# Kernel optimization log

Hardware: AMD Instinct MI355X
Metric: run time of the kernel (lower is better)

The kernel has to match this reference:

```python
import jax, jax.numpy as jnp
import numpy as np

D_MODEL, D_INNER, D_STATE, DT_RANK, D_CONV = 1024, 2048, 16, 64, 4
BATCH, SEQLEN = 2, 2048


def setup_inputs() -> dict:
    key = jax.random.key(0)
    ks = jax.random.split(key, 8)
    g = lambda k, shape, scale: jax.random.normal(k, shape, jnp.float32) * scale
    hidden_states = jax.random.normal(ks[0], (BATCH, SEQLEN, D_MODEL), jnp.float32)
    W_in = g(ks[1], (2 * D_INNER, D_MODEL), D_MODEL ** -0.5)
    conv_w = g(ks[2], (D_INNER, D_CONV), D_CONV ** -0.5)
    conv_b = jnp.zeros((D_INNER,), jnp.float32)
    W_x = g(ks[3], (DT_RANK + 2 * D_STATE, D_INNER), D_INNER ** -0.5)
    dt_init_std = DT_RANK ** -0.5  # dt_scale = 1.0
    W_dt = jax.random.uniform(ks[4], (D_INNER, DT_RANK), jnp.float32, -dt_init_std, dt_init_std)
    # faithful dt bias init: softplus^{-1}(dt) with dt ~ LogUniform(dt_min, dt_max)
    dt = jnp.exp(jax.random.uniform(ks[5], (D_INNER,), jnp.float32)
                 * (np.log(0.1) - np.log(0.001)) + np.log(0.001))
    dt = jnp.clip(dt, 1e-4)
    b_dt = dt + jnp.log(-jnp.expm1(-dt))
    A_log = jnp.log(jnp.broadcast_to(jnp.arange(1, D_STATE + 1, dtype=jnp.float32), (D_INNER, D_STATE)))
    D_param = jnp.ones((D_INNER,), jnp.float32)
    W_out = g(ks[6], (D_MODEL, D_INNER), D_INNER ** -0.5)
    return dict(hidden_states=hidden_states, W_in=W_in, conv_w=conv_w, conv_b=conv_b,
                W_x=W_x, W_dt=W_dt, b_dt=b_dt, A_log=A_log, D_param=D_param, W_out=W_out)


def reference(hidden_states, W_in, conv_w, conv_b, W_x, W_dt, b_dt, A_log, D_param, W_out):
    B_, L, _ = hidden_states.shape
    # in_proj (no bias) then split into x / gate z
    xz = jnp.einsum('bld,ed->ble', hidden_states, W_in)  # (B, L, 2*d_inner)
    x, z = jnp.split(xz, 2, axis=-1)
    # depthwise causal conv1d (padding = d_conv - 1, truncated to L)
    xp = jnp.pad(x, ((0, 0), (D_CONV - 1, 0), (0, 0)))
    xc = conv_b + sum(conv_w[:, k] * xp[:, k:k + L, :] for k in range(D_CONV))
    x = jax.nn.silu(xc)  # (B, L, d_inner)
    # input-dependent SSM params
    A = -jnp.exp(A_log)  # (d_inner, d_state)
    proj = jnp.einsum('bld,ed->ble', x, W_x)
    dt_lo, Bm, Cm = jnp.split(proj, [DT_RANK, DT_RANK + D_STATE], axis=-1)
    dt = jax.nn.softplus(jnp.einsum('blr,dr->bld', dt_lo, W_dt) + b_dt)  # (B, L, d_inner)
    # sequential selective scan: h = exp(dt*A)*h + dt*B*x ; y = C.h + D*x
    def step(h, inp):
        x_t, dt_t, B_t, C_t = inp  # (B,d), (B,d), (B,n), (B,n)
        dA = jnp.exp(dt_t[..., None] * A)                       # (B, d, n)
        h = dA * h + (dt_t * x_t)[..., None] * B_t[:, None, :]  # (B, d, n)
        y_t = jnp.einsum('bdn,bn->bd', h, C_t)
        return h, y_t

    h0 = jnp.zeros((B_, D_INNER, D_STATE), x.dtype)
    xs = (x.swapaxes(0, 1), dt.swapaxes(0, 1), Bm.swapaxes(0, 1), Cm.swapaxes(0, 1))
    _, ys = jax.lax.scan(step, h0, xs)
    y = ys.swapaxes(0, 1) + D_param * x
    y = y * jax.nn.silu(z)
    return jnp.einsum('bld,md->blm', y, W_out)
```

## Files before the change

### kernel.cpp

```cpp
#include <hip/hip_runtime.h>

typedef _Float16 f16;
typedef f16   f16x2 __attribute__((ext_vector_type(2)));
typedef f16   f16x4 __attribute__((ext_vector_type(4)));
typedef f16   f16x8 __attribute__((ext_vector_type(8)));
typedef float f32x2 __attribute__((ext_vector_type(2)));
typedef float f32x4 __attribute__((ext_vector_type(4)));

#define LOG2E 1.44269504088896f

__device__ __forceinline__ float fast_exp(float x) {
    return __builtin_amdgcn_exp2f(x * LOG2E);
}
__device__ __forceinline__ float silu_f(float x) {
    return x / (1.f + __builtin_amdgcn_exp2f(-LOG2E * x));
}
__device__ __forceinline__ float softplus_f(float x) {
    if (x > 16.f) return x;
    float e = __builtin_amdgcn_exp2f(x * LOG2E);
    return __builtin_amdgcn_logf(1.f + e) * 0.69314718056f;
}

__device__ __forceinline__ void gload_lds16(const void* g, void* l) {
    __builtin_amdgcn_global_load_lds((__attribute__((address_space(1))) void*)(g),
                                     (__attribute__((address_space(3))) void*)(l), 16, 0, 0);
}

__global__ __launch_bounds__(256) void cvt_all(const float* __restrict__ hidden, const float* __restrict__ W_in,
                                               const float* __restrict__ W_out, const float* __restrict__ W_dt,
                                               const float* __restrict__ W_x,
                                               f16* __restrict__ h16, f16* __restrict__ Win16,
                                               f16* __restrict__ Wout16, f16* __restrict__ Wdt16,
                                               f16* __restrict__ Wx16) {
    int i = blockIdx.x * 256 + threadIdx.x;
    const float* src;
    f16* dst;
    int idx;
    if (i < 1048576) { src = hidden; dst = h16; idx = i; }
    else if (i < 2097152) { src = W_in; dst = Win16; idx = i - 1048576; }
    else if (i < 2621440) { src = W_out; dst = Wout16; idx = i - 2097152; }
    else if (i < 2654208) { src = W_dt; dst = Wdt16; idx = i - 2621440; }
    else {
        int q = i - 2654208;
        int r = q >> 9;
        f32x4 v = {0.f, 0.f, 0.f, 0.f};
        if (r < 96) v = ((const f32x4*)W_x)[q];
        f16x4 o = {(f16)v[0], (f16)v[1], (f16)v[2], (f16)v[3]};
        ((f16x4*)Wx16)[q] = o;
        return;
    }
    f32x4 v = ((const f32x4*)src)[idx];
    f16x4 o = {(f16)v[0], (f16)v[1], (f16)v[2], (f16)v[3]};
    ((f16x4*)dst)[idx] = o;
}

__global__ void reduce_proj(const f16* __restrict__ Pws, float* __restrict__ proj,
                            f16* __restrict__ dtlo) {
    int i = blockIdx.x * 256 + threadIdx.x;
    int m = i >> 5, c0 = (i & 31) * 4;
    f32x4 s = {0.f, 0.f, 0.f, 0.f};
#pragma unroll
    for (int z = 0; z < 8; z++) {
        f16x4 p = *(const f16x4*)(Pws + (size_t)z * 4096 * 128 + (size_t)m * 128 + c0);
        s += (f32x4){(float)p[0], (float)p[1], (float)p[2], (float)p[3]};
    }
    *(f32x4*)(proj + (size_t)m * 128 + c0) = s;
    if (c0 < 64) {
        f16x4 o = {(f16)s[0], (f16)s[1], (f16)s[2], (f16)s[3]};
        *(f16x4*)(dtlo + (size_t)m * 64 + c0) = o;
    }
}

__global__ __launch_bounds__(1024) void gemm256(const f16* __restrict__ A, const f16* __restrict__ B,
                                                f16* __restrict__ C, int N, int K) {
    __shared__ f16 As[4][256 * 32];
    __shared__ f16 Bs[4][256 * 32];
    const int tid = threadIdx.x;
    const int w = tid >> 6, l = tid & 63;
    const int wr = w >> 2, wc = w & 3;
    const int lrow = l & 15, lkb = l >> 4;
    const int gpos = ((lkb ^ ((lrow >> 1) & 3)) * 8);
    const int bid = blockIdx.y * 16 + blockIdx.x;
    const int wg = (bid & 7) * 32 + (bid >> 3);
    const int mt = wg >> 4, nt = wg & 15;
    const int NT = K >> 5;

    f32x4 acc[4][4];
#pragma unroll
    for (int i = 0; i < 4; i++)
#pragma unroll
        for (int j = 0; j < 4; j++) acc[i][j] = (f32x4){0.f, 0.f, 0.f, 0.f};

    const int srow = w * 16 + (l >> 2);
    const int sgran = (l & 3) ^ ((l >> 3) & 3);
    const f16* Ag = A + (size_t)(mt * 256 + srow) * K + sgran * 8;
    const f16* Bg = B + (size_t)(nt * 256 + srow) * K + sgran * 8;

#define SCALL(s, kt, q)                                        \
    do {                                                       \
        if ((q) == 0) gload_lds16(Ag + (kt), &As[s][w * 512]); \
        if ((q) == 1) gload_lds16(Bg + (kt), &Bs[s][w * 512]); \
    } while (0)

    SCALL(0, 0, 0); SCALL(0, 0, 1);
    SCALL(1, 32, 0); SCALL(1, 32, 1);
    SCALL(2, 64, 0); SCALL(2, 64, 1);

    for (int t = 0; t < NT; ++t) {
        const f16* as = As[t & 3];
        const f16* bs = Bs[t & 3];
        const int pslot = (t + 3) & 3;
        const int pkt = ((t + 3 < NT) ? (t + 3) : (NT - 1)) * 32;

        asm volatile("s_waitcnt vmcnt(4)" ::: "memory");
        __builtin_amdgcn_sched_barrier(0);
        __builtin_amdgcn_s_barrier();
        __builtin_amdgcn_sched_barrier(0);

        f16x8 af[4], bf[4];
#pragma unroll
        for (int i = 0; i < 4; i++)
            af[i] = *(const f16x8*)&as[(wr * 64 + i * 16 + lrow) * 32 + gpos];
#pragma unroll
        for (int j = 0; j < 4; j++)
            bf[j] = *(const f16x8*)&bs[(wc * 64 + j * 16 + lrow) * 32 + gpos];
        SCALL(pslot, pkt, 0);
        SCALL(pslot, pkt, 1);
        __builtin_amdgcn_s_barrier();
        __builtin_amdgcn_sched_barrier(0);
        __builtin_amdgcn_s_setprio(1);
#pragma unroll
        for (int i = 0; i < 4; i++)
#pragma unroll
            for (int j = 0; j < 4; j++)
                acc[i][j] = __builtin_amdgcn_mfma_f32_16x16x32_f16(af[i], bf[j], acc[i][j], 0, 0, 0);
        __builtin_amdgcn_s_setprio(0);
    }
#undef SCALL

    const int orow = mt * 256 + wr * 64 + (l >> 4) * 4;
    const int ocol = nt * 256 + wc * 64 + lrow;
#pragma unroll
    for (int i = 0; i < 4; i++)
#pragma unroll
        for (int j = 0; j < 4; j++)
#pragma unroll
            for (int q = 0; q < 4; q++)
                C[(size_t)(orow + i * 16 + q) * N + ocol + j * 16] = (f16)acc[i][j][q];
}

__global__ __launch_bounds__(512) void gemm_o32(const f16* __restrict__ A, const f16* __restrict__ B,
                                                float* __restrict__ C, int N, int K) {
    __shared__ f16 As[4][128 * 32];
    __shared__ f16 Bs[4][128 * 32];
    const int tid = threadIdx.x;
    const int w = tid >> 6, l = tid & 63;
    const int wr = w >> 2, wc = w & 3;
    const int lrow = l & 15, lkb = l >> 4;
    const int gpos = ((lkb ^ ((lrow >> 1) & 3)) * 8);
    const int bid = blockIdx.y * 8 + blockIdx.x;
    const int wg = (bid & 7) * 32 + (bid >> 3);
    const int nt = wg & 7, mt = wg >> 3;
    const int NT = K >> 5;

    f32x4 acc[4][2];
#pragma unroll
    for (int i = 0; i < 4; i++)
#pragma unroll
        for (int j = 0; j < 2; j++) acc[i][j] = (f32x4){0.f, 0.f, 0.f, 0.f};

    const int srow = w * 16 + (l >> 2);
    const int sgran = (l & 3) ^ ((l >> 3) & 3);
    const f16* Ag = A + (size_t)(mt * 128 + srow) * K + sgran * 8;
    const f16* Bg = B + (size_t)(nt * 128 + srow) * K + sgran * 8;

#define QCALL(s, kt, q)                                        \
    do {                                                       \
        if ((q) == 0) gload_lds16(Ag + (kt), &As[s][w * 512]); \
        if ((q) == 1) gload_lds16(Bg + (kt), &Bs[s][w * 512]); \
    } while (0)

    QCALL(0, 0, 0); QCALL(0, 0, 1);
    QCALL(1, 32, 0); QCALL(1, 32, 1);
    QCALL(2, 64, 0); QCALL(2, 64, 1);

    for (int t = 0; t < NT; ++t) {
        const f16* as = As[t & 3];
        const f16* bs = Bs[t & 3];
        const int pslot = (t + 3) & 3;
        const int pkt = ((t + 3 < NT) ? (t + 3) : (NT - 1)) * 32;

        asm volatile("s_waitcnt vmcnt(4)" ::: "memory");
        __builtin_amdgcn_sched_barrier(0);
        __builtin_amdgcn_s_barrier();
        __builtin_amdgcn_sched_barrier(0);

        f16x8 af[4], bf[2];
#pragma unroll
        for (int i = 0; i < 4; i++)
            af[i] = *(const f16x8*)&as[(wr * 64 + i * 16 + lrow) * 32 + gpos];
#pragma unroll
        for (int j = 0; j < 2; j++)
            bf[j] = *(const f16x8*)&bs[(wc * 32 + j * 16 + lrow) * 32 + gpos];
        QCALL(pslot, pkt, 0);
        QCALL(pslot, pkt, 1);
        __builtin_amdgcn_s_barrier();
        __builtin_amdgcn_sched_barrier(0);
        __builtin_amdgcn_s_setprio(1);
#pragma unroll
        for (int i = 0; i < 4; i++)
#pragma unroll
            for (int j = 0; j < 2; j++)
                acc[i][j] = __builtin_amdgcn_mfma_f32_16x16x32_f16(af[i], bf[j], acc[i][j], 0, 0, 0);
        __builtin_amdgcn_s_setprio(0);
    }
#undef QCALL

    const int orow = mt * 128 + wr * 64 + (l >> 4) * 4;
    const int ocol = nt * 128 + wc * 32 + lrow;
#pragma unroll
    for (int i = 0; i < 4; i++)
#pragma unroll
        for (int j = 0; j < 2; j++)
#pragma unroll
            for (int q = 0; q < 4; q++)
                C[(size_t)(orow + i * 16 + q) * N + ocol + j * 16] = acc[i][j][q];
}

template <int EPI, typename OutT>
__global__ __launch_bounds__(256) void gemm_gl(const f16* __restrict__ A, const f16* __restrict__ B,
                                               OutT* __restrict__ C, const float* __restrict__ bias,
                                               int M, int N, int K, int kstep) {
    __shared__ f16 As[2][128 * 64];
    __shared__ f16 Bs[2][128 * 64];
    const int tid = threadIdx.x;
    const int w = tid >> 6, l = tid & 63;
    const int wm = (w >> 1) * 64, wn = (w & 1) * 64;
    const int lrow = l & 15, lkb = l >> 4;
    const int swzr = lrow & 7;
    const int gx = gridDim.x;
    const int nwg = gx * gridDim.y;
    const int bid = blockIdx.y * gx + blockIdx.x;
    const int wg = (bid & 7) * (nwg >> 3) + (bid >> 3);
    const int nt = wg % gx, mt = wg / gx;
    const int kbeg = blockIdx.z * kstep;
    const int NT = kstep >> 6;
    OutT* Cz = C + (size_t)blockIdx.z * M * N;

    f32x4 acc[4][4];
#pragma unroll
    for (int i = 0; i < 4; i++)
#pragma unroll
        for (int j = 0; j < 4; j++) acc[i][j] = (f32x4){0.f, 0.f, 0.f, 0.f};

    const int srow = w * 32 + (l >> 3);
    const int sgran = (l & 7) ^ (l >> 3);
    const f16* Ag = A + (size_t)(mt * 128 + srow) * K + sgran * 8 + kbeg;
    const f16* Bg = B + (size_t)(nt * 128 + srow) * K + sgran * 8 + kbeg;

#define STAGE128(s, kt)                                                         \
    do {                                                                        \
        _Pragma("unroll")                                                       \
        for (int i = 0; i < 4; ++i) {                                           \
            gload_lds16(Ag + (size_t)(i * 8) * K + (kt), &As[s][(w * 32 + i * 8) * 64]); \
            gload_lds16(Bg + (size_t)(i * 8) * K + (kt), &Bs[s][(w * 32 + i * 8) * 64]); \
        }                                                                       \
    } while (0)

    STAGE128(0, 0);
    __syncthreads();

    int cur = 0;
    for (int t = 0; t < NT; ++t) {
        if (t + 1 < NT) STAGE128(cur ^ 1, (t + 1) * 64);
#pragma unroll
        for (int kk = 0; kk < 64; kk += 32) {
            f16x8 af[4], bf[4];
            const int g = (kk >> 3) + lkb;
#pragma unroll
            for (int i = 0; i < 4; i++) {
                af[i] = *(const f16x8*)&As[cur][(wm + i * 16 + lrow) * 64 + ((g ^ swzr) * 8)];
                bf[i] = *(const f16x8*)&Bs[cur][(wn + i * 16 + lrow) * 64 + ((g ^ swzr) * 8)];
            }
#pragma unroll
            for (int i = 0; i < 4; i++)
#pragma unroll
                for (int j = 0; j < 4; j++)
                    acc[i][j] = __builtin_amdgcn_mfma_f32_16x16x32_f16(af[i], bf[j], acc[i][j], 0, 0, 0);
        }
        __syncthreads();
        cur ^= 1;
    }
#undef STAGE128

    const int orow = mt * 128 + wm + (l >> 4) * 4;
    const int ocol = nt * 128 + wn + lrow;
#pragma unroll
    for (int fm = 0; fm < 4; fm++)
#pragma unroll
        for (int fn = 0; fn < 4; fn++) {
            int c = ocol + fn * 16;
            float bv = (EPI == 1) ? bias[c] : 0.f;
#pragma unroll
            for (int i = 0; i < 4; i++) {
                float v = acc[fm][fn][i];
                if (EPI == 1) v = softplus_f(v + bv);
                Cz[(size_t)(orow + fm * 16 + i) * N + c] = (OutT)v;
            }
        }
}

__global__ __launch_bounds__(256) void conv_silu_k(const f16* __restrict__ xz, const float* __restrict__ cw,
                                                   const float* __restrict__ cb, f16* __restrict__ xc) {
    const int d0 = threadIdx.x * 8;
    const int g = blockIdx.x;
    const int b = g >> 9;
    const int l0 = (g & 511) * 4;
    const size_t mrow = (size_t)b * 2048 + l0;
    f32x4 cwv[8];
    float r0[8];
#pragma unroll
    for (int j = 0; j < 8; j++) {
        r0[j] = cb[d0 + j];
        cwv[j] = *(const f32x4*)(cw + (size_t)(d0 + j) * 4);
    }
    const f16x8 zero = {(f16)0.f, (f16)0.f, (f16)0.f, (f16)0.f, (f16)0.f, (f16)0.f, (f16)0.f, (f16)0.f};
    f16x8 xv[7];
#pragma unroll
    for (int i = 0; i < 7; ++i) {
        int ls = l0 - 3 + i;
        xv[i] = (ls >= 0) ? *(const f16x8*)(xz + (mrow - 3 + i) * 4096 + d0) : zero;
    }
#pragma unroll
    for (int tt = 0; tt < 4; ++tt) {
        float r[8];
#pragma unroll
        for (int j = 0; j < 8; j++) r[j] = r0[j];
#pragma unroll
        for (int k = 0; k < 4; k++)
#pragma unroll
            for (int j = 0; j < 8; j++) r[j] += cwv[j][k] * (float)xv[tt + k][j];
        f16x8 o;
#pragma unroll
        for (int j = 0; j < 8; j++) o[j] = (f16)silu_f(r[j]);
        *(f16x8*)(xc + (mrow + tt) * 2048 + d0) = o;
    }
}

#define CT 32
#define NCHUNK 64
#define NSTATE 65536

__global__ __launch_bounds__(64) void scan_p1(const f16* __restrict__ dt16, const f16* __restrict__ xc,
                                              const float* __restrict__ proj, const float* __restrict__ A_log,
                                              f16* __restrict__ Pbuf, f16* __restrict__ Hend) {
    __shared__ float du_s[CT][64];
    __shared__ float bq_s[CT][16];
    const int l = threadIdx.x;
    const int c = blockIdx.x, dgb = blockIdx.y, b = blockIdx.z;
    const int d_base = dgb << 6;
    const int d = d_base + l;
    const size_t mb = (size_t)b * 2048 + (size_t)c * CT;

    float a[16];
#pragma unroll
    for (int i = 0; i < 16; i += 4) {
        f32x4 av = *(const f32x4*)(A_log + (size_t)d * 16 + i);
#pragma unroll
        for (int k = 0; k < 4; ++k) a[i + k] = -fast_exp(av[k]) * LOG2E;
    }
#pragma unroll
    for (int i = 0; i < 4; ++i) {
        int idx = i * 64 + l, row = idx >> 3, j0 = (idx & 7) * 8;
        size_t r = mb + row;
        f16x8 dt8 = *(const f16x8*)(dt16 + r * 2048 + d_base + j0);
        f16x8 xc8 = *(const f16x8*)(xc + r * 2048 + d_base + j0);
#pragma unroll
        for (int k = 0; k < 8; ++k) {
            union { f16x2 h2; float f; } u;
            u.h2[0] = dt8[k];
            u.h2[1] = (f16)((float)dt8[k] * (float)xc8[k]);
            du_s[row][j0 + k] = u.f;
        }
    }
#pragma unroll
    for (int i = 0; i < 2; ++i) {
        int idx = i * 64 + l, row = idx >> 2, s4 = (idx & 3) * 4;
        *(f32x4*)&bq_s[row][s4] = *(const f32x4*)(proj + (mb + row) * 128 + 64 + s4);
    }
    __syncthreads();

    float h[16];
#pragma unroll
    for (int i = 0; i < 16; ++i) h[i] = 0.f;
    float sdt = 0.f;
#pragma unroll 2
    for (int t = 0; t < CT; ++t) {
        union { float f; f16x2 h2; } u;
        u.f = du_s[t][l];
        float dtv = (float)u.h2[0], uv = (float)u.h2[1];
        sdt += dtv;
        f32x4 B0 = *(const f32x4*)&bq_s[t][0];
        f32x4 B1 = *(const f32x4*)&bq_s[t][4];
        f32x4 B2 = *(const f32x4*)&bq_s[t][8];
        f32x4 B3 = *(const f32x4*)&bq_s[t][12];
#pragma unroll
        for (int i = 0; i < 4; ++i) {
            h[i]      = fmaf(__builtin_amdgcn_exp2f(dtv * a[i]),      h[i],      uv * B0[i]);
            h[i + 4]  = fmaf(__builtin_amdgcn_exp2f(dtv * a[i + 4]),  h[i + 4],  uv * B1[i]);
            h[i + 8]  = fmaf(__builtin_amdgcn_exp2f(dtv * a[i + 8]),  h[i + 8],  uv * B2[i]);
            h[i + 12] = fmaf(__builtin_amdgcn_exp2f(dtv * a[i + 12]), h[i + 12], uv * B3[i]);
        }
    }
    const size_t base = (size_t)c * NSTATE + ((size_t)((b << 11) + d) << 4);
    f16x8 P0, P1, E0, E1;
#pragma unroll
    for (int i = 0; i < 8; ++i) {
        P0[i] = (f16)__builtin_amdgcn_exp2f(a[i] * sdt);
        P1[i] = (f16)__builtin_amdgcn_exp2f(a[i + 8] * sdt);
        E0[i] = (f16)h[i];
        E1[i] = (f16)h[i + 8];
    }
    *(f16x8*)(Pbuf + base) = P0;
    *(f16x8*)(Pbuf + base + 8) = P1;
    *(f16x8*)(Hend + base) = E0;
    *(f16x8*)(Hend + base + 8) = E1;
}

__global__ __launch_bounds__(256) void scan_combine(const f16* __restrict__ Pbuf, const f16* __restrict__ Hend,
                                                    f16* __restrict__ Hinit) {
    int s = blockIdx.x * 256 + threadIdx.x;
    float h = 0.f;
#pragma unroll
    for (int c = 0; c < NCHUNK; c++) {
        size_t o = (size_t)c * NSTATE + s;
        Hinit[o] = (f16)h;
        h = fmaf((float)Pbuf[o], h, (float)Hend[o]);
    }
}

__global__ __launch_bounds__(64) void scan_p2(const f16* __restrict__ dt16, const f16* __restrict__ xc,
                                              const f16* __restrict__ xz, const float* __restrict__ proj,
                                              const float* __restrict__ A_log, const float* __restrict__ Dp,
                                              const f16* __restrict__ Hinit, f16* __restrict__ y16) {
    __shared__ f32x2 dg_s[CT][64];
    __shared__ float bq_s[CT][16];
    __shared__ float cq_s[CT][16];
    const int l = threadIdx.x;
    const int c = blockIdx.x, dgb = blockIdx.y, b = blockIdx.z;
    const int d_base = dgb << 6;
    const int d = d_base + l;
    const size_t mb = (size_t)b * 2048 + (size_t)c * CT;

    float a[16];
#pragma unroll
    for (int i = 0; i < 16; i += 4) {
        f32x4 av = *(const f32x4*)(A_log + (size_t)d * 16 + i);
#pragma unroll
        for (int k = 0; k < 4; ++k) a[i + k] = -fast_exp(av[k]) * LOG2E;
    }
#pragma unroll
    for (int i = 0; i < 4; ++i) {
        int idx = i * 64 + l, row = idx >> 3, j0 = (idx & 7) * 8;
        size_t r = mb + row;
        f16x8 dt8 = *(const f16x8*)(dt16 + r * 2048 + d_base + j0);
        f16x8 xc8 = *(const f16x8*)(xc + r * 2048 + d_base + j0);
        f16x8 xz8 = *(const f16x8*)(xz + r * 4096 + 2048 + d_base + j0);
        f32x4 dv0 = *(const f32x4*)(Dp + d_base + j0);
        f32x4 dv1 = *(const f32x4*)(Dp + d_base + j0 + 4);
#pragma unroll
        for (int k = 0; k < 8; ++k) {
            float dtv = (float)dt8[k], xv = (float)xc8[k];
            union { f16x2 h2; float f; } u;
            u.h2[0] = dt8[k];
            u.h2[1] = (f16)(dtv * xv);
            float sz = silu_f((float)xz8[k]);
            float Dv = (k < 4) ? dv0[k & 3] : dv1[k & 3];
            union { f16x2 h2; float f; } v;
            v.h2[0] = (f16)sz;
            v.h2[1] = (f16)(Dv * xv * sz);
            dg_s[row][j0 + k] = (f32x2){u.f, v.f};
        }
    }
#pragma unroll
    for (int i = 0; i < 2; ++i) {
        int idx = i * 64 + l, row = idx >> 2, s4 = (idx & 3) * 4;
        *(f32x4*)&bq_s[row][s4] = *(const f32x4*)(proj + (mb + row) * 128 + 64 + s4);
        *(f32x4*)&cq_s[row][s4] = *(const f32x4*)(proj + (mb + row) * 128 + 80 + s4);
    }
    const size_t base = (size_t)c * NSTATE + ((size_t)((b << 11) + d) << 4);
    f16x8 H0 = *(const f16x8*)(Hinit + base);
    f16x8 H1 = *(const f16x8*)(Hinit + base + 8);
    float h[16];
#pragma unroll
    for (int i = 0; i < 8; ++i) { h[i] = (float)H0[i]; h[i + 8] = (float)H1[i]; }
    __syncthreads();

#pragma unroll 2
    for (int t = 0; t < CT; ++t) {
        f32x2 dgv = dg_s[t][l];
        union { float f; f16x2 h2; } u;
        u.f = dgv[0];
        float dtv = (float)u.h2[0], uv = (float)u.h2[1];
        f32x4 B0 = *(const f32x4*)&bq_s[t][0];
        f32x4 B1 = *(const f32x4*)&bq_s[t][4];
        f32x4 B2 = *(const f32x4*)&bq_s[t][8];
        f32x4 B3 = *(const f32x4*)&bq_s[t][12];
        f32x4 C0 = *(const f32x4*)&cq_s[t][0];
        f32x4 C1 = *(const f32x4*)&cq_s[t][4];
        f32x4 C2 = *(const f32x4*)&cq_s[t][8];
        f32x4 C3 = *(const f32x4*)&cq_s[t][12];
        float yp0 = 0.f, yp1 = 0.f, yp2 = 0.f, yp3 = 0.f;
#pragma unroll
        for (int i = 0; i < 4; ++i) {
            h[i]      = fmaf(__builtin_amdgcn_exp2f(dtv * a[i]),      h[i],      uv * B0[i]);
            h[i + 4]  = fmaf(__builtin_amdgcn_exp2f(dtv * a[i + 4]),  h[i + 4],  uv * B1[i]);
            h[i + 8]  = fmaf(__builtin_amdgcn_exp2f(dtv * a[i + 8]),  h[i + 8],  uv * B2[i]);
            h[i + 12] = fmaf(__builtin_amdgcn_exp2f(dtv * a[i + 12]), h[i + 12], uv * B3[i]);
            yp0 = fmaf(h[i], C0[i], yp0);
            yp1 = fmaf(h[i + 4], C1[i], yp1);
            yp2 = fmaf(h[i + 8], C2[i], yp2);
            yp3 = fmaf(h[i + 12], C3[i], yp3);
        }
        float yp = (yp0 + yp1) + (yp2 + yp3);
        union { float f; f16x2 h2; } v;
        v.f = dgv[1];
        float yv = fmaf(yp, (float)v.h2[0], (float)v.h2[1]);
        y16[(mb + t) * 2048 + d] = (f16)yv;
    }
}

extern "C" void kernel_launch(void* const* d_in, const int* in_sizes, int n_in,
                              void* d_out, int out_size, void* d_ws, size_t ws_size,
                              hipStream_t stream) {
    const float* hidden = (const float*)d_in[0];
    const float* W_in   = (const float*)d_in[1];
    const float* conv_w = (const float*)d_in[2];
    const float* conv_b = (const float*)d_in[3];
    const float* W_x    = (const float*)d_in[4];
    const float* W_dt   = (const float*)d_in[5];
    const float* b_dt   = (const float*)d_in[6];
    const float* A_log  = (const float*)d_in[7];
    const float* D_par  = (const float*)d_in[8];
    const float* W_out  = (const float*)d_in[9];
    float* out = (float*)d_out;

    char* ws = (char*)d_ws;
    size_t off = 0;
    auto alloc = [&](size_t bytes) { void* p = ws + off; off += (bytes + 255) & ~(size_t)255; return p; };
    f16* h16     = (f16*)alloc(4096ull * 1024 * 2);
    f16* Win16   = (f16*)alloc(4096ull * 1024 * 2);
    f16* Wx16    = (f16*)alloc(128ull * 2048 * 2);
    f16* Wdt16   = (f16*)alloc(2048ull * 64 * 2);
    f16* Wout16  = (f16*)alloc(1024ull * 2048 * 2);
    f16* xz16    = (f16*)alloc(4096ull * 4096 * 2);
    f16* xc16    = (f16*)alloc(4096ull * 2048 * 2);
    float* proj  = (float*)alloc(4096ull * 128 * 4);
    f16* dtlo16  = (f16*)alloc(4096ull * 64 * 2);
    f16* dt16    = (f16*)alloc(4096ull * 2048 * 2);
    f16* y16     = (f16*)alloc(4096ull * 2048 * 2);
    f16* Pws     = (f16*)y16;
    f16* Pbuf16  = (f16*)h16;
    f16* Hend16  = (f16*)y16;
    f16* Hinit16 = (f16*)Win16;
    (void)ws_size; (void)in_sizes; (void)n_in; (void)out_size;

    cvt_all<<<10624, 256, 0, stream>>>(hidden, W_in, W_out, W_dt, W_x,
                                       h16, Win16, Wout16, Wdt16, Wx16);

    gemm256<<<dim3(16, 16), 1024, 0, stream>>>(h16, Win16, xz16, 4096, 1024);
    conv_silu_k<<<1024, 256, 0, stream>>>(xz16, conv_w, conv_b, xc16);
    gemm_gl<0, f16><<<dim3(1, 32, 8), 256, 0, stream>>>(xc16, Wx16, Pws, nullptr, 4096, 128, 2048, 256);
    reduce_proj<<<512, 256, 0, stream>>>(Pws, proj, dtlo16);
    gemm_gl<1, f16><<<dim3(16, 32, 1), 256, 0, stream>>>(dtlo16, Wdt16, dt16, b_dt, 4096, 2048, 64, 64);
    scan_p1<<<dim3(NCHUNK, 32, 2), 64, 0, stream>>>(dt16, xc16, proj, A_log, Pbuf16, Hend16);
    scan_combine<<<256, 256, 0, stream>>>(Pbuf16, Hend16, Hinit16);
    scan_p2<<<dim3(NCHUNK, 32, 2), 64, 0, stream>>>(dt16, xc16, xz16, proj, A_log, D_par, Hinit16, y16);
    gemm_o32<<<dim3(8, 32), 512, 0, stream>>>(y16, Wout16, out, 1024, 2048);
}
```

Baseline: 175.7 us.

## Split scan_p2 state dimension across 4 lanes with DPP reduction

Rewrites the second scan pass so each channel's 16 SSM states are spread over 4 lanes (4 states each), with blocks of 128 threads covering 32 channels and twice as many blocks in the grid. Partial C·h sums are combined across the 4 lanes with two DPP adds, and only one lane writes each output. This is meant to raise parallelism and occupancy and cut per-thread register pressure in the latency-bound recurrence. The cost is redundant exp/dt work and DPP overhead per lane, and only a quarter of the lanes doing the stores. It also pads the shared-memory arrays in both scan passes to reduce bank conflicts.

```diff
diff --git a/kernel.cpp b/kernel.cpp
--- a/kernel.cpp
+++ b/kernel.cpp
@@ -20,6 +20,9 @@
     float e = __builtin_amdgcn_exp2f(x * LOG2E);
     return __builtin_amdgcn_logf(1.f + e) * 0.69314718056f;
 }
+
+#define DPP_ADD(x, ctrl) \
+    ((x) + __int_as_float(__builtin_amdgcn_update_dpp(0, __float_as_int(x), (ctrl), 0xF, 0xF, true)))
 
 __device__ __forceinline__ void gload_lds16(const void* g, void* l) {
     __builtin_amdgcn_global_load_lds((__attribute__((address_space(1))) void*)(g),
@@ -354,7 +357,7 @@
 __global__ __launch_bounds__(64) void scan_p1(const f16* __restrict__ dt16, const f16* __restrict__ xc,
                                               const float* __restrict__ proj, const float* __restrict__ A_log,
                                               f16* __restrict__ Pbuf, f16* __restrict__ Hend) {
-    __shared__ float du_s[CT][64];
+    __shared__ float du_s[CT][66];
     __shared__ float bq_s[CT][16];
     const int l = threadIdx.x;
     const int c = blockIdx.x, dgb = blockIdx.y, b = blockIdx.z;
@@ -439,33 +442,31 @@
     }
 }
 
-__global__ __launch_bounds__(64) void scan_p2(const f16* __restrict__ dt16, const f16* __restrict__ xc,
-                                              const f16* __restrict__ xz, const float* __restrict__ proj,
-                                              const float* __restrict__ A_log, const float* __restrict__ Dp,
-                                              const f16* __restrict__ Hinit, f16* __restrict__ y16) {
-    __shared__ f32x2 dg_s[CT][64];
-    __shared__ float bq_s[CT][16];
-    __shared__ float cq_s[CT][16];
-    const int l = threadIdx.x;
-    const int c = blockIdx.x, dgb = blockIdx.y, b = blockIdx.z;
-    const int d_base = dgb << 6;
-    const int d = d_base + l;
+__global__ __launch_bounds__(128) void scan_p2(const f16* __restrict__ dt16, const f16* __restrict__ xc,
+                                               const f16* __restrict__ xz, const float* __restrict__ proj,
+                                               const float* __restrict__ A_log, const float* __restrict__ Dp,
+                                               const f16* __restrict__ Hinit, f16* __restrict__ y16) {
+    __shared__ f32x2 dg_s[CT][33];
+    __shared__ float bq_s[CT][20];
+    __shared__ float cq_s[CT][20];
+    const int tid = threadIdx.x;
+    const int c = blockIdx.x, dg = blockIdx.y, b = blockIdx.z;
+    const int d_base = dg << 5;
+    const int g = tid >> 2, n = tid & 3;
+    const int d = d_base + g;
+    f32x4 av = *(const f32x4*)(A_log + (size_t)d * 16 + n * 4);
+    const float a0 = -fast_exp(av[0]) * LOG2E;
+    const float a1 = -fast_exp(av[1]) * LOG2E;
+    const float a2 = -fast_exp(av[2]) * LOG2E;
+    const float a3 = -fast_exp(av[3]) * LOG2E;
     const size_t mb = (size_t)b * 2048 + (size_t)c * CT;
 
-    float a[16];
-#pragma unroll
-    for (int i = 0; i < 16; i += 4) {
-        f32x4 av = *(const f32x4*)(A_log + (size_t)d * 16 + i);
-#pragma unroll
-        for (int k = 0; k < 4; ++k) a[i + k] = -fast_exp(av[k]) * LOG2E;
-    }
-#pragma unroll
-    for (int i = 0; i < 4; ++i) {
-        int idx = i * 64 + l, row = idx >> 3, j0 = (idx & 7) * 8;
-        size_t r = mb + row;
-        f16x8 dt8 = *(const f16x8*)(dt16 + r * 2048 + d_base + j0);
-        f16x8 xc8 = *(const f16x8*)(xc + r * 2048 + d_base + j0);
-        f16x8 xz8 = *(const f16x8*)(xz + r * 4096 + 2048 + d_base + j0);
+    {
+        const int trow = tid >> 2, seg = tid & 3, j0 = seg * 8;
+        const size_t row = mb + trow;
+        f16x8 dt8 = *(const f16x8*)(dt16 + row * 2048 + d_base + j0);
+        f16x8 xc8 = *(const f16x8*)(xc + row * 2048 + d_base + j0);
+        f16x8 xz8 = *(const f16x8*)(xz + row * 4096 + 2048 + d_base + j0);
         f32x4 dv0 = *(const f32x4*)(Dp + d_base + j0);
         f32x4 dv1 = *(const f32x4*)(Dp + d_base + j0 + 4);
 #pragma unroll
@@ -479,54 +480,38 @@
             union { f16x2 h2; float f; } v;
             v.h2[0] = (f16)sz;
             v.h2[1] = (f16)(Dv * xv * sz);
-            dg_s[row][j0 + k] = (f32x2){u.f, v.f};
+            dg_s[trow][j0 + k] = (f32x2){u.f, v.f};
         }
-    }
-#pragma unroll
-    for (int i = 0; i < 2; ++i) {
-        int idx = i * 64 + l, row = idx >> 2, s4 = (idx & 3) * 4;
-        *(f32x4*)&bq_s[row][s4] = *(const f32x4*)(proj + (mb + row) * 128 + 64 + s4);
-        *(f32x4*)&cq_s[row][s4] = *(const f32x4*)(proj + (mb + row) * 128 + 80 + s4);
-    }
-    const size_t base = (size_t)c * NSTATE + ((size_t)((b << 11) + d) << 4);
-    f16x8 H0 = *(const f16x8*)(Hinit + base);
-    f16x8 H1 = *(const f16x8*)(Hinit + base + 8);
-    float h[16];
-#pragma unroll
-    for (int i = 0; i < 8; ++i) { h[i] = (float)H0[i]; h[i + 8] = (float)H1[i]; }
+        *(f32x4*)&bq_s[trow][seg * 4] = *(const f32x4*)(proj + row * 128 + 64 + seg * 4);
+        *(f32x4*)&cq_s[trow][seg * 4] = *(const f32x4*)(proj + row * 128 + 80 + seg * 4);
+    }
+    const size_t base = (size_t)c * NSTATE + ((size_t)((b << 11) + d) << 4) + n * 4;
+    f16x4 H4 = *(const f16x4*)(Hinit + base);
+    float h0 = (float)H4[0], h1 = (float)H4[1], h2 = (float)H4[2], h3 = (float)H4[3];
     __syncthreads();
 
-#pragma unroll 2
+#pragma unroll 8
     for (int t = 0; t < CT; ++t) {
-        f32x2 dgv = dg_s[t][l];
+        f32x2 dgv = dg_s[t][g];
         union { float f; f16x2 h2; } u;
         u.f = dgv[0];
         float dtv = (float)u.h2[0], uv = (float)u.h2[1];
-        f32x4 B0 = *(const f32x4*)&bq_s[t][0];
-        f32x4 B1 = *(const f32x4*)&bq_s[t][4];
-        f32x4 B2 = *(const f32x4*)&bq_s[t][8];
-        f32x4 B3 = *(const f32x4*)&bq_s[t][12];
-        f32x4 C0 = *(const f32x4*)&cq_s[t][0];
-        f32x4 C1 = *(const f32x4*)&cq_s[t][4];
-        f32x4 C2 = *(const f32x4*)&cq_s[t][8];
-        f32x4 C3 = *(const f32x4*)&cq_s[t][12];
-        float yp0 = 0.f, yp1 = 0.f, yp2 = 0.f, yp3 = 0.f;
-#pragma unroll
-        for (int i = 0; i < 4; ++i) {
-            h[i]      = fmaf(__builtin_amdgcn_exp2f(dtv * a[i]),      h[i],      uv * B0[i]);
-            h[i + 4]  = fmaf(__builtin_amdgcn_exp2f(dtv * a[i + 4]),  h[i + 4],  uv * B1[i]);
-            h[i + 8]  = fmaf(__builtin_amdgcn_exp2f(dtv * a[i + 8]),  h[i + 8],  uv * B2[i]);
-            h[i + 12] = fmaf(__builtin_amdgcn_exp2f(dtv * a[i + 12]), h[i + 12], uv * B3[i]);
-            yp0 = fmaf(h[i], C0[i], yp0);
-            yp1 = fmaf(h[i + 4], C1[i], yp1);
-            yp2 = fmaf(h[i + 8], C2[i], yp2);
-            yp3 = fmaf(h[i + 12], C3[i], yp3);
-        }
-        float yp = (yp0 + yp1) + (yp2 + yp3);
+        f32x4 B4 = *(const f32x4*)&bq_s[t][n * 4];
+        f32x4 C4 = *(const f32x4*)&cq_s[t][n * 4];
+        h0 = fmaf(__builtin_amdgcn_exp2f(dtv * a0), h0, uv * B4[0]);
+        h1 = fmaf(__builtin_amdgcn_exp2f(dtv * a1), h1, uv * B4[1]);
+        h2 = fmaf(__builtin_amdgcn_exp2f(dtv * a2), h2, uv * B4[2]);
+        h3 = fmaf(__builtin_amdgcn_exp2f(dtv * a3), h3, uv * B4[3]);
+        float yp = h0 * C4[0];
+        yp = fmaf(h1, C4[1], yp);
+        yp = fmaf(h2, C4[2], yp);
+        yp = fmaf(h3, C4[3], yp);
+        yp = DPP_ADD(yp, 0xB1);
+        yp = DPP_ADD(yp, 0x4E);
         union { float f; f16x2 h2; } v;
         v.f = dgv[1];
         float yv = fmaf(yp, (float)v.h2[0], (float)v.h2[1]);
-        y16[(mb + t) * 2048 + d] = (f16)yv;
+        if (n == 0) y16[(mb + t) * 2048 + d] = (f16)yv;
     }
 }
 
@@ -575,6 +560,6 @@
     gemm_gl<1, f16><<<dim3(16, 32, 1), 256, 0, stream>>>(dtlo16, Wdt16, dt16, b_dt, 4096, 2048, 64, 64);
     scan_p1<<<dim3(NCHUNK, 32, 2), 64, 0, stream>>>(dt16, xc16, proj, A_log, Pbuf16, Hend16);
     scan_combine<<<256, 256, 0, stream>>>(Pbuf16, Hend16, Hinit16);
-    scan_p2<<<dim3(NCHUNK, 32, 2), 64, 0, stream>>>(dt16, xc16, xz16, proj, A_log, D_par, Hinit16, y16);
+    scan_p2<<<dim3(NCHUNK, 64, 2), 128, 0, stream>>>(dt16, xc16, xz16, proj, A_log, D_par, Hinit16, y16);
     gemm_o32<<<dim3(8, 32), 512, 0, stream>>>(y16, Wout16, out, 1024, 2048);
 }
```

After: 179.9 us. +2.4%, slower.
